# Kernel tuning notes

Hardware: AMD Instinct MI355X
Metric: run time of the kernel (lower is better)

## Reference

```python
import jax, jax.numpy as jnp
import numpy as np

N = 8192
IN = 128   # in_channels
CH = 64    # conv_ch


def setup_inputs() -> dict:
    key = jax.random.key(0)
    ks = jax.random.split(key, 8)
    p = lambda k, shape: jax.random.normal(k, shape, jnp.float32) * 0.02
    return {
        "x": jax.random.normal(ks[0], (N, IN), jnp.float32),
        "edge_index": jax.random.randint(ks[1], (N, N), 0, 2, jnp.int32),
        "W1": p(ks[2], (IN, CH)),      "b1": jnp.zeros((CH,), jnp.float32),
        "W2": p(ks[3], (CH, 2 * CH)),  "b2": jnp.zeros((2 * CH,), jnp.float32),
        "We": p(ks[4], (2 * CH, CH)),  "be": jnp.zeros((CH,), jnp.float32),
        "Wd1": p(ks[5], (2 * CH, CH)), "bd1": jnp.zeros((CH,), jnp.float32),
        "Wd2": p(ks[6], (CH, IN)),     "bd2": jnp.zeros((IN,), jnp.float32),
    }


def _norm_adj(edge_index):
    # PyG GCNConv: A_hat = A + I (self loops appended), sym norm D^-1/2 A_hat D^-1/2
    A = (edge_index != 0).astype(jnp.float32)
    A = A + jnp.eye(A.shape[0], dtype=jnp.float32)
    deg = A.sum(axis=1)
    dinv = jnp.where(deg > 0.0, jax.lax.rsqrt(deg), 0.0)
    return dinv[:, None] * A * dinv[None, :]  # [N, N]


def _gcn(nadj, x, W, b):
    return nadj @ (x @ W) + b


def _lrelu(v):
    return jax.nn.leaky_relu(v, 0.01)  # torch default negative_slope


def reference(x, edge_index, W1, b1, W2, b2, We, be, Wd1, bd1, Wd2, bd2):
    nadj = _norm_adj(edge_index)
    h = _lrelu(_gcn(nadj, x, W1, b1))          # [N, CH]
    z = _lrelu(_gcn(nadj, h, W2, b2))          # [N, 2*CH]
    re = _lrelu(_gcn(nadj, z, We, be))         # [N, CH]
    recon_edge = jax.nn.sigmoid(re @ re.T)     # [N, N]
    xd = _lrelu(_gcn(nadj, z, Wd1, bd1))       # [N, CH]
    x_out = _lrelu(_gcn(nadj, xd, Wd2, bd2))   # [N, IN]
    return (recon_edge, x_out, z)
```

## Files before the change

### kernel.cpp

```cpp
#include <hip/hip_runtime.h>
#include <hip/hip_bf16.h>
#include <stdint.h>

typedef unsigned short u16;
typedef unsigned char u8;
typedef unsigned int u32;
typedef __attribute__((ext_vector_type(8))) short frag8;
typedef __attribute__((ext_vector_type(4))) float f4;

#define N8K 8192
#define SK 8
#define NKT 256


__device__ __forceinline__ u16 f2bf(float f) {
  union { float f; unsigned u; } v; v.f = f;
  return (u16)((v.u + 0x7FFFu + ((v.u >> 16) & 1u)) >> 16);
}
__device__ __forceinline__ float lrelu(float v) { return v > 0.f ? v : 0.01f * v; }

__device__ __forceinline__ void expand4(u32 w, u32& o0, u32& o1) {
  u32 hi = __builtin_amdgcn_perm(0u, 0x00403F00u, w);
  u32 lo = __builtin_amdgcn_perm(0u, 0x00008000u, w);
  o0 = __builtin_amdgcn_perm(hi, lo, 0x05010400u);
  o1 = __builtin_amdgcn_perm(hi, lo, 0x07030602u);
}

__global__ __launch_bounds__(256) void k_deg(const int* __restrict__ e,
                                             u8* __restrict__ at,
                                             float* __restrict__ dinv) {
  int Rt = blockIdx.x;
  int t = threadIdx.x;
  int rl = t & 15;
  int row = Rt * 16 + rl;
  int tg = t >> 4;
  int diagT = row >> 5;
  int cnt = 0;
  __shared__ int cs[256];
  for (int p = 0; p < 16; ++p) {
    int T = tg + 16 * p;
    const int4* src = (const int4*)(e + (size_t)row * N8K + T * 32);
    u32 w[8];
#pragma unroll
    for (int q8 = 0; q8 < 8; ++q8) {
      int4 v = src[q8];
      u32 c0 = (v.x != 0), c1 = (v.y != 0), c2 = (v.z != 0), c3 = (v.w != 0);
      cnt += (int)(c0 + c1 + c2 + c3);
      w[q8] = c0 | (c1 << 8) | (c2 << 16) | (c3 << 24);
    }
    if (T == diagT) {
      int d = row & 31;
      w[d >> 2] += 1u << (8 * (d & 3));
      cnt += 1;
    }
    u8* dst = at + ((size_t)(Rt * NKT + T) * 64 + rl) * 8;
#pragma unroll
    for (int q = 0; q < 4; ++q) {
      uint2 u; u.x = w[2 * q]; u.y = w[2 * q + 1];
      *(uint2*)(dst + (size_t)(16 * q) * 8) = u;
    }
  }
  cs[t] = cnt;
  __syncthreads();
  if (t < 16) {
    int s = 0;
#pragma unroll
    for (int g = 0; g < 16; ++g) s += cs[t + 16 * g];
    dinv[Rt * 16 + t] = 1.0f / sqrtf((float)s);
  }
}

__global__ __launch_bounds__(256, 2) void k_sgemm1(const float* __restrict__ Xf,
                                                   const float* __restrict__ Wa,
                                                   const float* __restrict__ dinv,
                                                   u16* __restrict__ Pt) {
  const int KT = 4;
  __shared__ __attribute__((aligned(16))) u16 Wt[8 * 4 * 64 * 8];
  int t = threadIdx.x, mt = blockIdx.x;
  int lane = t & 63, wave = t >> 6;
  for (int u = t; u < 8 * KT * 64; u += 256) {
    int l = u & 63, T = (u >> 6) % KT, nt = (u >> 6) / KT;
    int n = nt * 16 + (l & 15);
    int k0 = T * 32 + (l >> 4) * 8;
    u16 tmp[8];
#pragma unroll
    for (int j = 0; j < 8; ++j) {
      int k = k0 + j;
      float v = (n < 64) ? Wa[k * 64 + n] : 0.f;
      tmp[j] = f2bf(v);
    }
    *(uint4*)&Wt[(size_t)u * 8] = *(const uint4*)tmp;
  }
  __syncthreads();
  int wm = (wave >> 1) * 64, wn = (wave & 1) * 64;
  int fm = lane & 15, q = lane >> 4;
  f4 acc[4][4];
#pragma unroll
  for (int m = 0; m < 4; ++m)
#pragma unroll
    for (int n = 0; n < 4; ++n) acc[m][n] = (f4){0.f, 0.f, 0.f, 0.f};
  for (int T = 0; T < KT; ++T) {
    frag8 a[4], b[4];
#pragma unroll
    for (int m = 0; m < 4; ++m) {
      int Rt = mt * 8 + (wm >> 4) + m;
      const float* px = Xf + (size_t)(Rt * 16 + fm) * 128 + T * 32 + q * 8;
      float4 v0 = *(const float4*)px, v1 = *(const float4*)(px + 4);
      u16 tmp[8] = {f2bf(v0.x), f2bf(v0.y), f2bf(v0.z), f2bf(v0.w),
                    f2bf(v1.x), f2bf(v1.y), f2bf(v1.z), f2bf(v1.w)};
      a[m] = *(const frag8*)tmp;
    }
#pragma unroll
    for (int n = 0; n < 4; ++n)
      b[n] = *(const frag8*)&Wt[((size_t)(((wn >> 4) + n) * KT + T) * 64 + lane) * 8];
#pragma unroll
    for (int m = 0; m < 4; ++m)
#pragma unroll
      for (int n = 0; n < 4; ++n)
        acc[m][n] = __builtin_amdgcn_mfma_f32_16x16x32_bf16(a[m], b[n], acc[m][n], 0, 0, 0);
  }
#pragma unroll
  for (int m = 0; m < 4; ++m) {
    int ibase = mt * 128 + wm + 16 * m + q * 4;
    float d0 = dinv[ibase], d1 = dinv[ibase + 1], d2 = dinv[ibase + 2], d3 = dinv[ibase + 3];
#pragma unroll
    for (int n = 0; n < 4; ++n) {
      u32 lo = (u32)f2bf(d0 * acc[m][n][0]) | ((u32)f2bf(d1 * acc[m][n][1]) << 16);
      u32 hi = (u32)f2bf(d2 * acc[m][n][2]) | ((u32)f2bf(d3 * acc[m][n][3]) << 16);
      u32 plo = __shfl_xor(lo, 16, 64);
      u32 phi = __shfl_xor(hi, 16, 64);
      if ((q & 1) == 0) {
        uint4 u; u.x = lo; u.y = hi; u.z = plo; u.w = phi;
        int gi = mt * 128 + wm + 16 * m + (q >> 1) * 8;
        int T2 = gi >> 5;
        int lB = fm + 16 * ((gi >> 3) & 3);
        int nt = (wn >> 4) + n;
        *(uint4*)(Pt + ((size_t)(nt * NKT + T2) * 64 + lB) * 8) = u;
      }
    }
  }
}

__global__ __launch_bounds__(256, 3) void k_bgemm(const u8* __restrict__ At,
                                                  const u16* __restrict__ Bt,
                                                  float* __restrict__ Ctmp) {
  int t = threadIdx.x;
  int mt = blockIdx.x, ks = blockIdx.y;
  int lane = t & 63, wave = t >> 6;
  int wm = (wave >> 1) * 64, wn = (wave & 1) * 64;
  f4 acc[4][4];
#pragma unroll
  for (int m = 0; m < 4; ++m)
#pragma unroll
    for (int n = 0; n < 4; ++n) acc[m][n] = (f4){0.f, 0.f, 0.f, 0.f};

  const int T0 = ks * 32;
  const u8*  Ab = At + ((size_t)((mt * 8 + (wm >> 4)) * NKT + T0) * 64 + lane) * 8;
  const u16* Bb = Bt + ((size_t)(((wn >> 4)) * NKT + T0) * 64 + lane) * 8;

#pragma unroll 2
  for (int T = 0; T < 32; ++T) {
    frag8 a[4], b[4];
#pragma unroll
    for (int m = 0; m < 4; ++m) {
      uint2 w = *(const uint2*)(Ab + (size_t)m * (NKT * 512) + (size_t)T * 512);
      uint4 r;
      expand4(w.x, r.x, r.y);
      expand4(w.y, r.z, r.w);
      a[m] = *(const frag8*)&r;
    }
#pragma unroll
    for (int n = 0; n < 4; ++n)
      b[n] = *(const frag8*)(Bb + (size_t)n * (NKT * 512) + (size_t)T * 512);
#pragma unroll
    for (int m = 0; m < 4; ++m)
#pragma unroll
      for (int n = 0; n < 4; ++n)
        acc[m][n] = __builtin_amdgcn_mfma_f32_16x16x32_bf16(a[m], b[n], acc[m][n], 0, 0, 0);
  }

  float* Co = Ctmp + (size_t)ks * (N8K * 128);
  int fm = lane & 15, rbase = (lane >> 4) * 4;
#pragma unroll
  for (int m = 0; m < 4; ++m) {
    int i0 = mt * 128 + wm + 16 * m + rbase;
#pragma unroll
    for (int n = 0; n < 4; ++n) {
      int c = wn + 16 * n + fm;
#pragma unroll
      for (int r = 0; r < 4; ++r) Co[(size_t)(i0 + r) * 128 + c] = acc[m][n][r];
    }
  }
}

__global__ __launch_bounds__(256, 2) void k_fuse(const float* __restrict__ Ctmp,
                                                 const float* __restrict__ dinv,
                                                 const float* __restrict__ bE,
                                                 const float* __restrict__ bE2,
                                                 float* __restrict__ outZ,
                                                 u16* __restrict__ retG,
                                                 int mode,
                                                 const float* __restrict__ Wa, int wacols,
                                                 const float* __restrict__ Wb,
                                                 u16* __restrict__ Pt) {
  __shared__ __attribute__((aligned(16))) u16 Xs[8 * 4 * 64 * 8];
  __shared__ __attribute__((aligned(16))) u16 Wt[8 * 4 * 64 * 8];
  int t = threadIdx.x, mt = blockIdx.x;
  int lane = t & 63, wave = t >> 6;
  const int KT = (mode == 2) ? 4 : 2;

  int C8 = (mode == 1) ? 8 : 16;
  int totalU = 128 * C8;
  for (int u0 = t; u0 < totalU; u0 += 256) {
    int i = (mode == 1) ? (u0 >> 3) : (u0 >> 4);
    int c8 = (mode == 1) ? (u0 & 7) : (u0 & 15);
    int gi = mt * 128 + i;
    int c0 = c8 * 8;
    float v[8];
#pragma unroll
    for (int j = 0; j < 8; ++j) v[j] = 0.f;
#pragma unroll
    for (int k = 0; k < SK; ++k) {
      const float4* p = (const float4*)(Ctmp + (size_t)k * (N8K * 128) + (size_t)gi * 128 + c0);
      float4 x0 = p[0], x1 = p[1];
      v[0] += x0.x; v[1] += x0.y; v[2] += x0.z; v[3] += x0.w;
      v[4] += x1.x; v[5] += x1.y; v[6] += x1.z; v[7] += x1.w;
    }
    float di = dinv[gi];
    u16 ob[8];
    if (mode == 3 && c8 < 8) {
#pragma unroll
      for (int j = 0; j < 8; ++j) ob[j] = f2bf(lrelu(di * v[j] + bE[c0 + j]));
      int T = c8 >> 2, l = (i & 15) + 16 * (c8 & 3);
      *(uint4*)(retG + ((size_t)((gi >> 4) * 2 + T) * 64 + l) * 8) = *(const uint4*)ob;
    } else if (mode == 3) {
      int cl = c0 - 64;
#pragma unroll
      for (int j = 0; j < 8; ++j) ob[j] = f2bf(lrelu(di * v[j] + bE2[cl + j]));
      int cp = c8 - 8;
      int T = cp >> 2, l = (i & 15) + 16 * (cp & 3);
      *(uint4*)&Xs[(((i >> 4) * 2 + T) * 64 + l) * 8] = *(const uint4*)ob;
    } else {
#pragma unroll
      for (int j = 0; j < 8; ++j) v[j] = lrelu(di * v[j] + bE[c0 + j]);
#pragma unroll
      for (int j = 0; j < 8; ++j) ob[j] = f2bf(v[j]);
      int T = c8 >> 2, l = (i & 15) + 16 * (c8 & 3);
      *(uint4*)&Xs[(((i >> 4) * KT + T) * 64 + l) * 8] = *(const uint4*)ob;
      if (mode == 2) {
        float4* po = (float4*)(outZ + (size_t)gi * 128 + c0);
        po[0] = (float4){v[0], v[1], v[2], v[3]};
        po[1] = (float4){v[4], v[5], v[6], v[7]};
      }
    }
  }

  for (int u = t; u < 8 * KT * 64; u += 256) {
    int l = u & 63, T = (u >> 6) % KT, nt = (u >> 6) / KT;
    int n = nt * 16 + (l & 15);
    int k0 = T * 32 + (l >> 4) * 8;
    u16 tmp[8];
#pragma unroll
    for (int j = 0; j < 8; ++j) {
      int k = k0 + j;
      float v = (n < wacols) ? Wa[k * wacols + n] : (Wb ? Wb[k * 64 + (n - 64)] : 0.f);
      tmp[j] = f2bf(v);
    }
    *(uint4*)&Wt[(size_t)u * 8] = *(const uint4*)tmp;
  }
  __syncthreads();

  int wm = (wave >> 1) * 64, wn = (wave & 1) * 64;
  int fm = lane & 15, q = lane >> 4;
  f4 acc[4][4];
#pragma unroll
  for (int m = 0; m < 4; ++m)
#pragma unroll
    for (int n = 0; n < 4; ++n) acc[m][n] = (f4){0.f, 0.f, 0.f, 0.f};
  for (int T = 0; T < KT; ++T) {
    frag8 a[4], b[4];
#pragma unroll
    for (int m = 0; m < 4; ++m)
      a[m] = *(const frag8*)&Xs[((size_t)(((wm >> 4) + m) * KT + T) * 64 + lane) * 8];
#pragma unroll
    for (int n = 0; n < 4; ++n)
      b[n] = *(const frag8*)&Wt[((size_t)(((wn >> 4) + n) * KT + T) * 64 + lane) * 8];
#pragma unroll
    for (int m = 0; m < 4; ++m)
#pragma unroll
      for (int n = 0; n < 4; ++n)
        acc[m][n] = __builtin_amdgcn_mfma_f32_16x16x32_bf16(a[m], b[n], acc[m][n], 0, 0, 0);
  }
#pragma unroll
  for (int m = 0; m < 4; ++m) {
    int ibase = mt * 128 + wm + 16 * m + q * 4;
    float d0 = dinv[ibase], d1 = dinv[ibase + 1], d2 = dinv[ibase + 2], d3 = dinv[ibase + 3];
#pragma unroll
    for (int n = 0; n < 4; ++n) {
      u32 lo = (u32)f2bf(d0 * acc[m][n][0]) | ((u32)f2bf(d1 * acc[m][n][1]) << 16);
      u32 hi = (u32)f2bf(d2 * acc[m][n][2]) | ((u32)f2bf(d3 * acc[m][n][3]) << 16);
      u32 plo = __shfl_xor(lo, 16, 64);
      u32 phi = __shfl_xor(hi, 16, 64);
      if ((q & 1) == 0) {
        uint4 u; u.x = lo; u.y = hi; u.z = plo; u.w = phi;
        int gi = mt * 128 + wm + 16 * m + (q >> 1) * 8;
        int T2 = gi >> 5;
        int lB = fm + 16 * ((gi >> 3) & 3);
        int nt = (wn >> 4) + n;
        *(uint4*)(Pt + ((size_t)(nt * NKT + T2) * 64 + lB) * 8) = u;
      }
    }
  }
}

__global__ __launch_bounds__(256) void k_epi4(const float* __restrict__ Ctmp,
                                              const float* __restrict__ dinv,
                                              const float* __restrict__ bA,
                                              float* __restrict__ outF) {
  int idx = blockIdx.x * 256 + threadIdx.x;
  int i = idx >> 4, c8 = idx & 15;
  int c0 = c8 * 8;
  float v[8];
#pragma unroll
  for (int j = 0; j < 8; ++j) v[j] = 0.f;
#pragma unroll
  for (int k = 0; k < SK; ++k) {
    const float4* p = (const float4*)(Ctmp + (size_t)k * (N8K * 128) + (size_t)i * 128 + c0);
    float4 x0 = p[0], x1 = p[1];
    v[0] += x0.x; v[1] += x0.y; v[2] += x0.z; v[3] += x0.w;
    v[4] += x1.x; v[5] += x1.y; v[6] += x1.z; v[7] += x1.w;
  }
  float di = dinv[i];
#pragma unroll
  for (int j = 0; j < 8; ++j) v[j] = lrelu(di * v[j] + bA[c0 + j]);
  float4* po = (float4*)(outF + (size_t)i * 128 + c0);
  po[0] = (float4){v[0], v[1], v[2], v[3]};
  po[1] = (float4){v[4], v[5], v[6], v[7]};
}

__global__ __launch_bounds__(256, 4) void k_recon(const u16* __restrict__ ret,
                                                  float* __restrict__ out) {
  int t = threadIdx.x;
  int bi = blockIdx.x, bj = blockIdx.y;
  int lane = t & 63, wave = t >> 6;
  int wm = (wave >> 1) * 64, wn = (wave & 1) * 64;
  int fm = lane & 15;
  f4 acc[4][4];
#pragma unroll
  for (int m = 0; m < 4; ++m)
#pragma unroll
    for (int n = 0; n < 4; ++n) acc[m][n] = (f4){0.f, 0.f, 0.f, 0.f};
#pragma unroll
  for (int T = 0; T < 2; ++T) {
    frag8 a[4], b[4];
#pragma unroll
    for (int m = 0; m < 4; ++m)
      a[m] = *(const frag8*)(ret + ((size_t)((bi * 8 + (wm >> 4) + m) * 2 + T) * 64 + lane) * 8);
#pragma unroll
    for (int n = 0; n < 4; ++n)
      b[n] = *(const frag8*)(ret + ((size_t)((bj * 8 + (wn >> 4) + n) * 2 + T) * 64 + lane) * 8);
#pragma unroll
    for (int m = 0; m < 4; ++m)
#pragma unroll
      for (int n = 0; n < 4; ++n)
        acc[m][n] = __builtin_amdgcn_mfma_f32_16x16x32_bf16(a[m], b[n], acc[m][n], 0, 0, 0);
  }
  int rbase = (lane >> 4) * 4;
#pragma unroll
  for (int m = 0; m < 4; ++m) {
#pragma unroll
    for (int n = 0; n < 4; ++n) {
      int gj = bj * 128 + wn + 16 * n + fm;
#pragma unroll
      for (int r = 0; r < 4; ++r) {
        int gi = bi * 128 + wm + 16 * m + rbase + r;
        float ex = __builtin_amdgcn_exp2f(acc[m][n][r] * -1.442695041f);
        out[(size_t)gi * N8K + gj] = __builtin_amdgcn_rcpf(1.0f + ex);
      }
    }
  }
}

extern "C" void kernel_launch(void* const* d_in, const int* in_sizes, int n_in,
                              void* d_out, int out_size, void* d_ws, size_t ws_size,
                              hipStream_t stream) {
  const float* x   = (const float*)d_in[0];
  const int*   e   = (const int*)d_in[1];
  const float* W1  = (const float*)d_in[2];
  const float* b1  = (const float*)d_in[3];
  const float* W2  = (const float*)d_in[4];
  const float* b2  = (const float*)d_in[5];
  const float* We  = (const float*)d_in[6];
  const float* be  = (const float*)d_in[7];
  const float* Wd1 = (const float*)d_in[8];
  const float* bd1 = (const float*)d_in[9];
  const float* Wd2 = (const float*)d_in[10];
  const float* bd2 = (const float*)d_in[11];

  float* out       = (float*)d_out;
  float* out_recon = out;
  float* out_x     = out + 67108864;
  float* out_z     = out + 67108864 + 1048576;

  u8*    at   = (u8*)d_out;
  float* Ctmp = out + 16777216;

  char* ws = (char*)d_ws;
  float* dinv = (float*)(ws);
  u16* Pt  = (u16*)(ws + 32768);
  u16* ret = (u16*)(ws + 32768 + 2097152);

  k_deg<<<512, 256, 0, stream>>>(e, at, dinv);

  k_sgemm1<<<64, 256, 0, stream>>>(x, W1, dinv, Pt);
  k_bgemm<<<dim3(64, SK), 256, 0, stream>>>(at, Pt, Ctmp);

  k_fuse<<<64, 256, 0, stream>>>(Ctmp, dinv, b1, nullptr, nullptr, nullptr, 1,
                                 W2, 128, nullptr, Pt);
  k_bgemm<<<dim3(64, SK), 256, 0, stream>>>(at, Pt, Ctmp);

  k_fuse<<<64, 256, 0, stream>>>(Ctmp, dinv, b2, nullptr, out_z, nullptr, 2,
                                 We, 64, Wd1, Pt);
  k_bgemm<<<dim3(64, SK), 256, 0, stream>>>(at, Pt, Ctmp);

  k_fuse<<<64, 256, 0, stream>>>(Ctmp, dinv, be, bd1, nullptr, ret, 3,
                                 Wd2, 128, nullptr, Pt);
  k_bgemm<<<dim3(64, SK), 256, 0, stream>>>(at, Pt, Ctmp);

  k_epi4<<<512, 256, 0, stream>>>(Ctmp, dinv, bd2, out_x);

  k_recon<<<dim3(64, 64), 256, 0, stream>>>(ret, out_recon);
}
```

Before: 687.8 us.

## Pack adjacency into 2-bit entries and halve split-K in binary GEMM

Packs the adjacency (A+I) matrix at 2 bits per entry instead of 8, so the repeated sparse-dense GEMM passes read a quarter as many bytes of adjacency data. The bgemm kernel now unpacks each 32-bit word into two bf16 fragments covering 64 columns and issues two MFMA batches per step. Split-K drops from 8 to 4, which shrinks the partial-sum buffer traffic. The launch bound drops to 1 block per CU, so fewer blocks run at once and per-CU occupancy is lower.

```diff
diff --git a/kernel.cpp b/kernel.cpp
--- a/kernel.cpp
+++ b/kernel.cpp
@@ -9,8 +9,9 @@
 typedef __attribute__((ext_vector_type(4))) float f4;
 
 #define N8K 8192
-#define SK 8
+#define SK 4
 #define NKT 256
+#define NT2 128
 
 
 __device__ __forceinline__ u16 f2bf(float f) {
@@ -25,6 +26,9 @@
   o0 = __builtin_amdgcn_perm(hi, lo, 0x05010400u);
   o1 = __builtin_amdgcn_perm(hi, lo, 0x07030602u);
 }
+
+#define WQ(col) (((col) & 31) >> 3)
+#define SHIFT(col) (8 * (((col) & 7) & 3) + 2 * (((col) & 7) >> 2) + 4 * ((col) >> 5))
 
 __global__ __launch_bounds__(256) void k_deg(const int* __restrict__ e,
                                              u8* __restrict__ at,
@@ -34,31 +38,37 @@
   int rl = t & 15;
   int row = Rt * 16 + rl;
   int tg = t >> 4;
-  int diagT = row >> 5;
+  int diagT2 = row >> 6;
   int cnt = 0;
   __shared__ int cs[256];
-  for (int p = 0; p < 16; ++p) {
-    int T = tg + 16 * p;
-    const int4* src = (const int4*)(e + (size_t)row * N8K + T * 32);
-    u32 w[8];
-#pragma unroll
-    for (int q8 = 0; q8 < 8; ++q8) {
+  for (int p = 0; p < 8; ++p) {
+    int T2 = tg + 16 * p;
+    const int4* src = (const int4*)(e + (size_t)row * N8K + T2 * 64);
+    u32 w[4] = {0u, 0u, 0u, 0u};
+#pragma unroll
+    for (int q8 = 0; q8 < 16; ++q8) {
       int4 v = src[q8];
       u32 c0 = (v.x != 0), c1 = (v.y != 0), c2 = (v.z != 0), c3 = (v.w != 0);
       cnt += (int)(c0 + c1 + c2 + c3);
-      w[q8] = c0 | (c1 << 8) | (c2 << 16) | (c3 << 24);
-    }
-    if (T == diagT) {
-      int d = row & 31;
-      w[d >> 2] += 1u << (8 * (d & 3));
+      const int cb = q8 * 4;
+      w[WQ(cb + 0)] |= c0 << SHIFT(cb + 0);
+      w[WQ(cb + 1)] |= c1 << SHIFT(cb + 1);
+      w[WQ(cb + 2)] |= c2 << SHIFT(cb + 2);
+      w[WQ(cb + 3)] |= c3 << SHIFT(cb + 3);
+    }
+    if (T2 == diagT2) {
+      int col = row & 63;
+      int qd = (col & 31) >> 3;
+      u32 add = 1u << (8 * ((col & 7) & 3) + 2 * ((col & 7) >> 2) + 4 * (col >> 5));
+#pragma unroll
+      for (int q = 0; q < 4; ++q)
+        if (q == qd) w[q] += add;
       cnt += 1;
     }
-    u8* dst = at + ((size_t)(Rt * NKT + T) * 64 + rl) * 8;
-#pragma unroll
-    for (int q = 0; q < 4; ++q) {
-      uint2 u; u.x = w[2 * q]; u.y = w[2 * q + 1];
-      *(uint2*)(dst + (size_t)(16 * q) * 8) = u;
-    }
+    u8* dst = at + ((size_t)(Rt * NT2 + T2) * 64 + rl) * 4;
+#pragma unroll
+    for (int q = 0; q < 4; ++q)
+      *(u32*)(dst + (size_t)(16 * q) * 4) = w[q];
   }
   cs[t] = cnt;
   __syncthreads();
@@ -141,7 +151,7 @@
   }
 }
 
-__global__ __launch_bounds__(256, 3) void k_bgemm(const u8* __restrict__ At,
+__global__ __launch_bounds__(256, 1) void k_bgemm(const u8* __restrict__ At,
                                                   const u16* __restrict__ Bt,
                                                   float* __restrict__ Ctmp) {
   int t = threadIdx.x;
@@ -154,29 +164,44 @@
 #pragma unroll
     for (int n = 0; n < 4; ++n) acc[m][n] = (f4){0.f, 0.f, 0.f, 0.f};
 
-  const int T0 = ks * 32;
-  const u8*  Ab = At + ((size_t)((mt * 8 + (wm >> 4)) * NKT + T0) * 64 + lane) * 8;
-  const u16* Bb = Bt + ((size_t)(((wn >> 4)) * NKT + T0) * 64 + lane) * 8;
+  const int T20 = ks * 32;
+  const u8*  Ab = At + ((size_t)((mt * 8 + (wm >> 4)) * NT2 + T20) * 64 + lane) * 4;
+  const u16* Bb = Bt + ((size_t)(((wn >> 4)) * NKT + 2 * T20) * 64 + lane) * 8;
 
 #pragma unroll 2
-  for (int T = 0; T < 32; ++T) {
-    frag8 a[4], b[4];
+  for (int T2 = 0; T2 < 32; ++T2) {
+    u32 w[4];
+    frag8 aE[4], aO[4], bE[4], bO[4];
+#pragma unroll
+    for (int m = 0; m < 4; ++m)
+      w[m] = *(const u32*)(Ab + (size_t)m * (NT2 * 256) + (size_t)T2 * 256);
+#pragma unroll
+    for (int n = 0; n < 4; ++n) {
+      bE[n] = *(const frag8*)(Bb + (size_t)n * (NKT * 512) + (size_t)(2 * T2) * 512);
+      bO[n] = *(const frag8*)(Bb + (size_t)n * (NKT * 512) + (size_t)(2 * T2) * 512 + 512);
+    }
 #pragma unroll
     for (int m = 0; m < 4; ++m) {
-      uint2 w = *(const uint2*)(Ab + (size_t)m * (NKT * 512) + (size_t)T * 512);
-      uint4 r;
-      expand4(w.x, r.x, r.y);
-      expand4(w.y, r.z, r.w);
-      a[m] = *(const frag8*)&r;
-    }
-#pragma unroll
-    for (int n = 0; n < 4; ++n)
-      b[n] = *(const frag8*)(Bb + (size_t)n * (NKT * 512) + (size_t)T * 512);
+      u32 e0 = w[m] & 0x03030303u;
+      u32 e1 = (w[m] >> 2) & 0x03030303u;
+      u32 e2 = (w[m] >> 4) & 0x03030303u;
+      u32 e3 = (w[m] >> 6) & 0x03030303u;
+      uint4 rE, rO;
+      expand4(e0, rE.x, rE.y); expand4(e1, rE.z, rE.w);
+      expand4(e2, rO.x, rO.y); expand4(e3, rO.z, rO.w);
+      aE[m] = *(const frag8*)&rE;
+      aO[m] = *(const frag8*)&rO;
+    }
 #pragma unroll
     for (int m = 0; m < 4; ++m)
 #pragma unroll
       for (int n = 0; n < 4; ++n)
-        acc[m][n] = __builtin_amdgcn_mfma_f32_16x16x32_bf16(a[m], b[n], acc[m][n], 0, 0, 0);
+        acc[m][n] = __builtin_amdgcn_mfma_f32_16x16x32_bf16(aE[m], bE[n], acc[m][n], 0, 0, 0);
+#pragma unroll
+    for (int m = 0; m < 4; ++m)
+#pragma unroll
+      for (int n = 0; n < 4; ++n)
+        acc[m][n] = __builtin_amdgcn_mfma_f32_16x16x32_bf16(aO[m], bO[n], acc[m][n], 0, 0, 0);
   }
 
   float* Co = Ctmp + (size_t)ks * (N8K * 128);
```

After: 655.4 us. -4.7%, faster.
